# Performance work log

Measured on AMD Instinct MI355X. Metric: run time of the kernel, lower is better.

The kernel has to match this reference:

```python
import jax, jax.numpy as jnp
import numpy as np

B, H, W, C = 2, 128, 128, 256
D = 64          # attention_dim
NH = 1          # num_heads
P = 18          # num_random_points
N = H * W
EPS = 1e-5


def _layernorm(x, gamma, beta):
    mu = jnp.mean(x, axis=-1, keepdims=True)
    var = jnp.var(x, axis=-1, keepdims=True)
    return (x - mu) * jax.lax.rsqrt(var + EPS) * gamma + beta


def setup_inputs() -> dict:
    key = jax.random.key(0)
    ks = jax.random.split(key, 12)
    s = 0.02
    inp = {
        "X": jax.random.normal(ks[0], (B, H, W, C), dtype=jnp.float32),
        "selected_indices": jax.random.randint(ks[1], (B, N, P), 0, N),
        "topk": 1,
        "pos_enc": jax.random.normal(ks[2], (1, H, W, C), dtype=jnp.float32),
        "Wq": jax.random.normal(ks[3], (C, NH * D), dtype=jnp.float32) * s,
        "bq": jnp.zeros((NH * D,), dtype=jnp.float32),
        "Wk": jax.random.normal(ks[4], (C, NH * D), dtype=jnp.float32) * s,
        "bk": jnp.zeros((NH * D,), dtype=jnp.float32),
        "Wv": jax.random.normal(ks[5], (C, NH * D), dtype=jnp.float32) * s,
        "bv": jnp.zeros((NH * D,), dtype=jnp.float32),
        "Wo": jax.random.normal(ks[6], (NH * D, C), dtype=jnp.float32) * s,
        "bo": jnp.zeros((C,), dtype=jnp.float32),
        "W1": jax.random.normal(ks[7], (C, 4 * C), dtype=jnp.float32) * s,
        "b1": jnp.zeros((4 * C,), dtype=jnp.float32),
        "W2": jax.random.normal(ks[8], (4 * C, C), dtype=jnp.float32) * s,
        "b2": jnp.zeros((C,), dtype=jnp.float32),
        "g1": jnp.ones((C,), dtype=jnp.float32),
        "be1": jnp.zeros((C,), dtype=jnp.float32),
        "g2": jnp.ones((C,), dtype=jnp.float32),
        "be2": jnp.zeros((C,), dtype=jnp.float32),
    }
    return inp


def reference(X, selected_indices, topk, pos_enc, Wq, bq, Wk, bk, Wv, bv,
              Wo, bo, W1, b1, W2, b2, g1, be1, g2, be2):
    # forward_wotopk path (topk == 1)
    Xp = X + pos_enc                                  # [B,H,W,C]
    Q = (Xp @ Wq + bq).reshape(B, N, NH, D)
    K = (Xp @ Wk + bk).reshape(B, N, NH, D)
    V = (Xp @ Wv + bv).reshape(B, N, NH, D)

    # gather 18 random K/V rows per query pixel: [B,N,P,NH,D]
    gather = jax.vmap(lambda kv, idx: kv[idx])        # per-batch fancy index
    Ksel = gather(K, selected_indices)
    Vsel = gather(V, selected_indices)

    scores = jnp.einsum('bihd,bijhd->bijh', Q, Ksel) / jnp.sqrt(
        jnp.asarray(D, dtype=jnp.float32))
    attn = jax.nn.softmax(scores, axis=2)             # softmax over the P points
    ctx = jnp.einsum('bijh,bijhd->bihd', attn, Vsel).reshape(B, N, NH * D)

    out = (ctx @ Wo + bo).reshape(B, H, W, C)
    Xn = _layernorm(Xp + out, g1, be1)
    ffn = jax.nn.relu(Xn @ W1 + b1) @ W2 + b2
    out2 = _layernorm(Xn + ffn, g2, be2)
    return out2, attn
```

## Files before the change

### kernel.cpp

```cpp
#include <hip/hip_runtime.h>
#include <hip/hip_bf16.h>

#define CC 256
#define DD 64
#define PP 18
#define ROWS 32768
#define EPSF 1e-5f

typedef __attribute__((ext_vector_type(8))) short bf16x8;
typedef __attribute__((ext_vector_type(4))) short s16x4;
typedef __attribute__((ext_vector_type(4))) float f32x4;

__global__ __launch_bounds__(256) void k_prep(
    const float* __restrict__ Wq, const float* __restrict__ Wk,
    const float* __restrict__ Wv, const float* __restrict__ Wo,
    const float* __restrict__ W1, const float* __restrict__ W2,
    __hip_bfloat16* __restrict__ WqP, __hip_bfloat16* __restrict__ WkP,
    __hip_bfloat16* __restrict__ WvP, __hip_bfloat16* __restrict__ WoP,
    __hip_bfloat16* __restrict__ W1T, __hip_bfloat16* __restrict__ W2T) {
    __shared__ float tile[32][33];
    const int b = blockIdx.x, t = threadIdx.x;
    if (b < 256) {
        int i = b * 256 + t;
        const float* src; __hip_bfloat16* dst; int K, N, j;
        if (i < 16384)      { src = Wq; dst = WqP; K = 256; N = 64;  j = i; }
        else if (i < 32768) { src = Wk; dst = WkP; K = 256; N = 64;  j = i - 16384; }
        else if (i < 49152) { src = Wv; dst = WvP; K = 256; N = 64;  j = i - 32768; }
        else                { src = Wo; dst = WoP; K = 64;  N = 256; j = i - 49152; }
        int e = j & 7, l = (j >> 3) & 63, rest = j >> 9;
        int KS = K >> 5;
        int ks = rest % KS, nt = rest / KS;
        int row = ks * 32 + (l >> 4) * 8 + e;
        int col = nt * 16 + (l & 15);
        dst[j] = __float2bfloat16(src[(long)row * N + col]);
        return;
    }
    const float* src; __hip_bfloat16* dst; int Nsrc, r0, c0, mode;
    if (b < 512) {
        int bb = b - 256;
        r0 = (bb >> 5) * 32; c0 = (bb & 31) * 32;
        src = W1; dst = W1T; Nsrc = 1024; mode = 0;
    } else {
        int bb = b - 512;
        r0 = (bb >> 3) * 32; c0 = (bb & 7) * 32;
        src = W2; dst = W2T; Nsrc = 256; mode = 1;
    }
#pragma unroll
    for (int i = 0; i < 4; ++i) {
        int idx = t + i * 256;
        int r = idx >> 5, c = idx & 31;
        tile[r][c] = src[(long)(r0 + r) * Nsrc + c0 + c];
    }
    __syncthreads();
#pragma unroll
    for (int i = 0; i < 4; ++i) {
        int idx = t + i * 256;
        int c2 = idx >> 5, r2 = idx & 31;
        long doff = (mode == 0) ? ((long)(c0 + c2) * 256 + r0 + r2)
                                : ((long)(c0 + c2) * 1024 + r0 + r2);
        dst[doff] = __float2bfloat16(tile[r2][c2]);
    }
}

__global__ __launch_bounds__(256) void k_qkv(
    const float4* __restrict__ X4, const float4* __restrict__ pe4,
    const __hip_bfloat16* __restrict__ WqP, const __hip_bfloat16* __restrict__ WkP,
    const __hip_bfloat16* __restrict__ WvP,
    const float* __restrict__ bq, const float* __restrict__ bk,
    const float* __restrict__ bv,
    __hip_bfloat16* __restrict__ Xpb,
    __hip_bfloat16* __restrict__ Qb, __hip_bfloat16* __restrict__ Kb,
    __hip_bfloat16* __restrict__ Vb) {
    __shared__ short Xs[32 * 256];
    const int t = threadIdx.x, w = t >> 6, l = t & 63;
    const int l15 = l & 15, lh = l >> 4;
    const int row0 = blockIdx.x * 32;

    for (int j = t; j < 2048; j += 256) {
        int r = j >> 6, c4 = j & 63;
        long g = row0 + r;
        float4 a = X4[(g << 6) + c4];
        float4 p = pe4[(long)((g & 16383) << 6) + c4];
        union { s16x4 v; __hip_bfloat16 h[4]; } u;
        u.h[0] = __float2bfloat16(a.x + p.x);
        u.h[1] = __float2bfloat16(a.y + p.y);
        u.h[2] = __float2bfloat16(a.z + p.z);
        u.h[3] = __float2bfloat16(a.w + p.w);
        int db = (r << 9) + (c4 << 3);
        db ^= (r & 7) << 4;
        *(s16x4*)((char*)Xs + db) = u.v;
        *(s16x4*)((char*)Xpb + (g << 9) + (c4 << 3)) = u.v;
    }
    __syncthreads();

    bf16x8 af[2][8];
#pragma unroll
    for (int ri = 0; ri < 2; ++ri)
#pragma unroll
        for (int ks = 0; ks < 8; ++ks) {
            int r = ri * 16 + l15;
            int db = (r << 9) + ks * 64 + lh * 16;
            db ^= (r & 7) << 4;
            af[ri][ks] = *(const bf16x8*)((const char*)Xs + db);
        }

    f32x4 acc[3][2];
#pragma unroll
    for (int j = 0; j < 3; ++j)
#pragma unroll
        for (int ri = 0; ri < 2; ++ri) acc[j][ri] = (f32x4)(0.f);

#pragma unroll
    for (int ks = 0; ks < 8; ++ks)
#pragma unroll
        for (int j = 0; j < 3; ++j) {
            int nt = w * 3 + j;
            const __hip_bfloat16* WP = (nt < 4) ? WqP : ((nt < 8) ? WkP : WvP);
            int ntl = nt & 3;
            bf16x8 b = *(const bf16x8*)(WP + (long)(((ntl * 8 + ks) << 6) + l) * 8);
#pragma unroll
            for (int ri = 0; ri < 2; ++ri)
                acc[j][ri] = __builtin_amdgcn_mfma_f32_16x16x32_bf16(
                    af[ri][ks], b, acc[j][ri], 0, 0, 0);
        }

#pragma unroll
    for (int j = 0; j < 3; ++j) {
        int nt = w * 3 + j;
        __hip_bfloat16* OP = (nt < 4) ? Qb : ((nt < 8) ? Kb : Vb);
        const float* BP = (nt < 4) ? bq : ((nt < 8) ? bk : bv);
        int col = (nt & 3) * 16 + l15;
        float bias = BP[col];
#pragma unroll
        for (int ri = 0; ri < 2; ++ri)
#pragma unroll
            for (int rg = 0; rg < 4; ++rg) {
                long row = row0 + ri * 16 + lh * 4 + rg;
                OP[row * DD + col] = __float2bfloat16(acc[j][ri][rg] + bias);
            }
    }
}

__global__ __launch_bounds__(256) void k_attn(const __hip_bfloat16* __restrict__ Q,
                                              const __hip_bfloat16* __restrict__ K,
                                              const __hip_bfloat16* __restrict__ V,
                                              const int* __restrict__ sel,
                                              __hip_bfloat16* __restrict__ ctx,
                                              float* __restrict__ attn_out) {
    const int wave  = threadIdx.x >> 6;
    const int lane  = threadIdx.x & 63;
    const int token = blockIdx.x * 4 + wave;
    const int b     = token >> 14;
    const int g = lane >> 3, s = lane & 7;

    const int* selp = sel + (long)token * PP;
    int sel_l = (lane < PP) ? selp[lane] : 0;

    float qf[8];
    {
        uint4 qv = *(const uint4*)(Q + (long)token * DD + s * 8);
        qf[0] = __uint_as_float(qv.x << 16);
        qf[1] = __uint_as_float(qv.x & 0xffff0000u);
        qf[2] = __uint_as_float(qv.y << 16);
        qf[3] = __uint_as_float(qv.y & 0xffff0000u);
        qf[4] = __uint_as_float(qv.z << 16);
        qf[5] = __uint_as_float(qv.z & 0xffff0000u);
        qf[6] = __uint_as_float(qv.w << 16);
        qf[7] = __uint_as_float(qv.w & 0xffff0000u);
    }

    const __hip_bfloat16* Kbase = K + (((long)b << 14) * DD);
    float sc[3];
    int idxs[3];
#pragma unroll
    for (int i = 0; i < 3; ++i) {
        int r = i * 8 + g;
        idxs[i] = __shfl(sel_l, r);
        uint4 kv = *(const uint4*)(Kbase + (long)idxs[i] * DD + s * 8);
        float part;
        part = qf[0] * __uint_as_float(kv.x << 16);
        part = fmaf(qf[1], __uint_as_float(kv.x & 0xffff0000u), part);
        part = fmaf(qf[2], __uint_as_float(kv.y << 16), part);
        part = fmaf(qf[3], __uint_as_float(kv.y & 0xffff0000u), part);
        part = fmaf(qf[4], __uint_as_float(kv.z << 16), part);
        part = fmaf(qf[5], __uint_as_float(kv.z & 0xffff0000u), part);
        part = fmaf(qf[6], __uint_as_float(kv.w << 16), part);
        part = fmaf(qf[7], __uint_as_float(kv.w & 0xffff0000u), part);
        part += __shfl_xor(part, 1);
        part += __shfl_xor(part, 2);
        part += __shfl_xor(part, 4);
        sc[i] = (r < PP) ? part * 0.125f : -1e30f;
    }

    float m = fmaxf(fmaxf(sc[0], sc[1]), sc[2]);
    m = fmaxf(m, __shfl_xor(m, 8));
    m = fmaxf(m, __shfl_xor(m, 16));
    m = fmaxf(m, __shfl_xor(m, 32));
    const float L2E = 1.4426950408889634f;
    float e0 = exp2f((sc[0] - m) * L2E);
    float e1 = exp2f((sc[1] - m) * L2E);
    float e2 = exp2f((sc[2] - m) * L2E);
    float dsum = e0 + e1 + e2;
    dsum += __shfl_xor(dsum, 8);
    dsum += __shfl_xor(dsum, 16);
    dsum += __shfl_xor(dsum, 32);
    float inv = 1.f / dsum;

    {
        int srcl = (lane & 7) << 3;
        float b0 = __shfl(e0, srcl);
        float b1 = __shfl(e1, srcl);
        float b2 = __shfl(e2, srcl);
        if (lane < PP) {
            float ev = (lane < 8) ? b0 : ((lane < 16) ? b1 : b2);
            attn_out[(long)token * PP + lane] = ev * inv;
        }
    }

    const __hip_bfloat16* Vbase = V + (((long)b << 14) * DD);
    float ca[8];
#pragma unroll
    for (int j = 0; j < 8; ++j) ca[j] = 0.f;
    float ev3[3] = {e0, e1, e2};
#pragma unroll
    for (int i = 0; i < 3; ++i) {
        uint4 vv = *(const uint4*)(Vbase + (long)idxs[i] * DD + s * 8);
        float e = ev3[i];
        ca[0] = fmaf(e, __uint_as_float(vv.x << 16), ca[0]);
        ca[1] = fmaf(e, __uint_as_float(vv.x & 0xffff0000u), ca[1]);
        ca[2] = fmaf(e, __uint_as_float(vv.y << 16), ca[2]);
        ca[3] = fmaf(e, __uint_as_float(vv.y & 0xffff0000u), ca[3]);
        ca[4] = fmaf(e, __uint_as_float(vv.z << 16), ca[4]);
        ca[5] = fmaf(e, __uint_as_float(vv.z & 0xffff0000u), ca[5]);
        ca[6] = fmaf(e, __uint_as_float(vv.w << 16), ca[6]);
        ca[7] = fmaf(e, __uint_as_float(vv.w & 0xffff0000u), ca[7]);
    }
#pragma unroll
    for (int o = 8; o <= 32; o <<= 1)
#pragma unroll
        for (int j = 0; j < 8; ++j) ca[j] += __shfl_xor(ca[j], o);
    if (g == 0) {
        union { bf16x8 v; __hip_bfloat16 h[8]; } u;
#pragma unroll
        for (int j = 0; j < 8; ++j) u.h[j] = __float2bfloat16(ca[j] * inv);
        *(bf16x8*)(ctx + (long)token * DD + s * 8) = u.v;
    }
}

__global__ __launch_bounds__(256) void k_projln(
    const __hip_bfloat16* __restrict__ ctx, const __hip_bfloat16* __restrict__ WoP,
    const float* __restrict__ bo, const float* __restrict__ g1,
    const float* __restrict__ be1,
    const __hip_bfloat16* __restrict__ Xpb, __hip_bfloat16* __restrict__ Xnb) {
    __shared__ short Cs[32 * 64];
    __shared__ float red[2][32][2];
    __shared__ float mrs[32][2];
    const int t = threadIdx.x, w = t >> 6, l = t & 63;
    const int l15 = l & 15, lh = l >> 4;
    const int row0 = blockIdx.x * 32;

    {
        int r = t >> 3, ch = t & 7;
        int db = (r << 7) + (ch << 4);
        db ^= (r & 7) << 4;
        *(bf16x8*)((char*)Cs + db) = *(const bf16x8*)(ctx + (long)(row0 + r) * DD + ch * 8);
    }
    __syncthreads();

    const int ri = w & 1, nh = w >> 1;

    bf16x8 af[2];
#pragma unroll
    for (int ks = 0; ks < 2; ++ks) {
        int r = ri * 16 + l15;
        int db = (r << 7) + ks * 64 + lh * 16;
        db ^= (r & 7) << 4;
        af[ks] = *(const bf16x8*)((const char*)Cs + db);
    }

    f32x4 acc[8];
#pragma unroll
    for (int j = 0; j < 8; ++j) acc[j] = (f32x4)(0.f);

#pragma unroll
    for (int ks = 0; ks < 2; ++ks)
#pragma unroll
        for (int j = 0; j < 8; ++j) {
            int nt = nh * 8 + j;
            bf16x8 b = *(const bf16x8*)(WoP + (long)(((nt * 2 + ks) << 6) + l) * 8);
            acc[j] = __builtin_amdgcn_mfma_f32_16x16x32_bf16(af[ks], b, acc[j], 0, 0, 0);
        }

    float bov[8], g1v[8], be1v[8];
#pragma unroll
    for (int j = 0; j < 8; ++j) {
        int col = (nh * 8 + j) * 16 + l15;
        bov[j] = bo[col]; g1v[j] = g1[col]; be1v[j] = be1[col];
    }

    float xv[4][8];
#pragma unroll
    for (int rg = 0; rg < 4; ++rg) {
        long grow = row0 + ri * 16 + lh * 4 + rg;
        float s = 0.f, q = 0.f;
#pragma unroll
        for (int j = 0; j < 8; ++j) {
            float v = acc[j][rg] + bov[j] +
                      __bfloat162float(Xpb[grow * CC + (nh * 8 + j) * 16 + l15]);
            xv[rg][j] = v; s += v; q += v * v;
        }
#pragma unroll
        for (int o = 8; o > 0; o >>= 1) { s += __shfl_xor(s, o); q += __shfl_xor(q, o); }
        if (l15 == 0) {
            int rl = ri * 16 + lh * 4 + rg;
            red[nh][rl][0] = s; red[nh][rl][1] = q;
        }
    }
    __syncthreads();
    if (t < 32) {
        float S = red[0][t][0] + red[1][t][0];
        float Q = red[0][t][1] + red[1][t][1];
        float mu = S * (1.f / CC);
        float var = Q * (1.f / CC) - mu * mu;
        mrs[t][0] = mu; mrs[t][1] = rsqrtf(var + EPSF);
    }
    __syncthreads();
#pragma unroll
    for (int rg = 0; rg < 4; ++rg) {
        int rl = ri * 16 + lh * 4 + rg;
        long grow = row0 + rl;
        float mu = mrs[rl][0], rs = mrs[rl][1];
#pragma unroll
        for (int j = 0; j < 8; ++j)
            Xnb[grow * CC + (nh * 8 + j) * 16 + l15] =
                __float2bfloat16((xv[rg][j] - mu) * rs * g1v[j] + be1v[j]);
    }
}

template<int KD, int NDIM, int GRL2, int CTL2>
__global__ __launch_bounds__(256) void k_gemm(
    const __hip_bfloat16* __restrict__ A,
    const __hip_bfloat16* __restrict__ BT,
    const float* __restrict__ bias,
    __hip_bfloat16* __restrict__ Cout) {
    __shared__ short As[4096];
    __shared__ short Bs[4096];

    const int t = threadIdx.x, w = t >> 6, l = t & 63;
    const int l15 = l & 15, lh = l >> 4;
    const int bid = blockIdx.x;
    const int wi = bid & ((1 << (GRL2 + CTL2)) - 1);
    const int rt = ((bid >> (GRL2 + CTL2)) << GRL2) | (wi & ((1 << GRL2) - 1));
    const int ct = wi >> GRL2;
    const int row0 = rt * 128, n0 = ct * 128;
    const int wr = w & 1, wc = w >> 1;

    const int ar = t >> 2;
    const int ak = (t & 3) << 3;
    const int dbase = (ar * 64 + ((t & 3) << 4)) ^ ((ar & 7) << 4);
    const __hip_bfloat16* Ap = A + (long)(row0 + ar) * KD + ak;
    const __hip_bfloat16* Bp = BT + (long)(n0 + ar) * KD + ak;

    bf16x8 ra0 = *(const bf16x8*)(Ap);
    bf16x8 ra1 = *(const bf16x8*)(Ap + (long)64 * KD);
    bf16x8 rb0 = *(const bf16x8*)(Bp);
    bf16x8 rb1 = *(const bf16x8*)(Bp + (long)64 * KD);

    int offA[4], offB[4];
#pragma unroll
    for (int f = 0; f < 4; ++f) {
        int rowA = wr * 64 + f * 16 + l15;
        offA[f] = (rowA * 64 + lh * 16) ^ ((rowA & 7) << 4);
        int rowB = wc * 64 + f * 16 + l15;
        offB[f] = (rowB * 64 + lh * 16) ^ ((rowB & 7) << 4);
    }

    f32x4 acc[4][4];
#pragma unroll
    for (int i = 0; i < 4; ++i)
#pragma unroll
        for (int j = 0; j < 4; ++j) acc[i][j] = (f32x4)(0.f);

    constexpr int KS = KD / 32;
#pragma unroll 1
    for (int ks = 0; ks < KS; ++ks) {
        __syncthreads();
        *(bf16x8*)((char*)As + dbase)        = ra0;
        *(bf16x8*)((char*)As + 4096 + dbase) = ra1;
        *(bf16x8*)((char*)Bs + dbase)        = rb0;
        *(bf16x8*)((char*)Bs + 4096 + dbase) = rb1;
        if (ks + 1 < KS) {
            const __hip_bfloat16* Ap2 = Ap + (ks + 1) * 32;
            const __hip_bfloat16* Bp2 = Bp + (ks + 1) * 32;
            ra0 = *(const bf16x8*)(Ap2);
            ra1 = *(const bf16x8*)(Ap2 + (long)64 * KD);
            rb0 = *(const bf16x8*)(Bp2);
            rb1 = *(const bf16x8*)(Bp2 + (long)64 * KD);
        }
        __syncthreads();
        bf16x8 af[4], bfr[4];
#pragma unroll
        for (int f = 0; f < 4; ++f)
            af[f] = *(const bf16x8*)((const char*)As + offA[f]);
#pragma unroll
        for (int f = 0; f < 4; ++f)
            bfr[f] = *(const bf16x8*)((const char*)Bs + offB[f]);
#pragma unroll
        for (int fr = 0; fr < 4; ++fr)
#pragma unroll
            for (int fc = 0; fc < 4; ++fc)
                acc[fr][fc] = __builtin_amdgcn_mfma_f32_16x16x32_bf16(
                    af[fr], bfr[fc], acc[fr][fc], 0, 0, 0);
    }

#pragma unroll
    for (int fc = 0; fc < 4; ++fc) {
        int col = n0 + wc * 64 + fc * 16 + l15;
        float bv = bias[col];
#pragma unroll
        for (int fr = 0; fr < 4; ++fr)
#pragma unroll
            for (int rg = 0; rg < 4; ++rg) {
                int row = wr * 64 + fr * 16 + lh * 4 + rg;
                long gi = (long)(row0 + row) * NDIM + col;
                Cout[gi] = __float2bfloat16(fmaxf(acc[fr][fc][rg] + bv, 0.f));
            }
    }
}

__global__ __launch_bounds__(512) void k_gemm2ln(
    const __hip_bfloat16* __restrict__ A,
    const __hip_bfloat16* __restrict__ BT,
    const float* __restrict__ b2,
    const __hip_bfloat16* __restrict__ Res,
    const float* __restrict__ g2, const float* __restrict__ be2,
    float* __restrict__ out) {
    __shared__ short As[4096];
    __shared__ short Bs[8192];
    __shared__ float red[4][128][2];
    __shared__ float mrs[128][2];

    const int t = threadIdx.x, w = t >> 6, l = t & 63;
    const int l15 = l & 15, lh = l >> 4;
    const int wr = w >> 2, wc = w & 3;
    const int row0 = blockIdx.x * 128;

    const int ar = t >> 2;
    const int ak = (t & 3) << 3;
    const int dbA  = (ar * 64 + ((t & 3) << 4)) ^ ((ar & 7) << 4);
    const int br1  = ar + 128;
    const int dbB0 = dbA;
    const int dbB1 = (br1 * 64 + ((t & 3) << 4)) ^ ((br1 & 7) << 4);
    const __hip_bfloat16* Ap  = A  + (long)(row0 + ar) * 1024 + ak;
    const __hip_bfloat16* Bp0 = BT + (long)ar  * 1024 + ak;
    const __hip_bfloat16* Bp1 = BT + (long)br1 * 1024 + ak;

    bf16x8 ra  = *(const bf16x8*)(Ap);
    bf16x8 rb0 = *(const bf16x8*)(Bp0);
    bf16x8 rb1 = *(const bf16x8*)(Bp1);

    int offA[4], offB[4];
#pragma unroll
    for (int f = 0; f < 4; ++f) {
        int rowA = wr * 64 + f * 16 + l15;
        offA[f] = (rowA * 64 + lh * 16) ^ ((rowA & 7) << 4);
        int rowB = wc * 64 + f * 16 + l15;
        offB[f] = (rowB * 64 + lh * 16) ^ ((rowB & 7) << 4);
    }

    f32x4 acc[4][4];
#pragma unroll
    for (int i = 0; i < 4; ++i)
#pragma unroll
        for (int j = 0; j < 4; ++j) acc[i][j] = (f32x4)(0.f);

#pragma unroll 1
    for (int ks = 0; ks < 32; ++ks) {
        __syncthreads();
        *(bf16x8*)((char*)As + dbA)  = ra;
        *(bf16x8*)((char*)Bs + dbB0) = rb0;
        *(bf16x8*)((char*)Bs + dbB1) = rb1;
        if (ks + 1 < 32) {
            ra  = *(const bf16x8*)(Ap  + (ks + 1) * 32);
            rb0 = *(const bf16x8*)(Bp0 + (ks + 1) * 32);
            rb1 = *(const bf16x8*)(Bp1 + (ks + 1) * 32);
        }
        __syncthreads();
        bf16x8 af[4], bfr[4];
#pragma unroll
        for (int f = 0; f < 4; ++f)
            af[f] = *(const bf16x8*)((const char*)As + offA[f]);
#pragma unroll
        for (int f = 0; f < 4; ++f)
            bfr[f] = *(const bf16x8*)((const char*)Bs + offB[f]);
#pragma unroll
        for (int fr = 0; fr < 4; ++fr)
#pragma unroll
            for (int fc = 0; fc < 4; ++fc)
                acc[fr][fc] = __builtin_amdgcn_mfma_f32_16x16x32_bf16(
                    af[fr], bfr[fc], acc[fr][fc], 0, 0, 0);
    }

    float b2v[4], g2v[4], be2v[4];
#pragma unroll
    for (int fc = 0; fc < 4; ++fc) {
        int col = wc * 64 + fc * 16 + l15;
        b2v[fc] = b2[col]; g2v[fc] = g2[col]; be2v[fc] = be2[col];
    }
#pragma unroll
    for (int fr = 0; fr < 4; ++fr)
#pragma unroll
        for (int rg = 0; rg < 4; ++rg) {
            int row = wr * 64 + fr * 16 + lh * 4 + rg;
            float s = 0.f, q = 0.f;
#pragma unroll
            for (int fc = 0; fc < 4; ++fc) {
                long gi = (long)(row0 + row) * CC + wc * 64 + fc * 16 + l15;
                float v = acc[fr][fc][rg] + b2v[fc] + __bfloat162float(Res[gi]);
                acc[fr][fc][rg] = v;
                s += v; q += v * v;
            }
#pragma unroll
            for (int o = 8; o > 0; o >>= 1) {
                s += __shfl_xor(s, o); q += __shfl_xor(q, o);
            }
            if (l15 == 0) { red[wc][row][0] = s; red[wc][row][1] = q; }
        }
    __syncthreads();
    if (t < 128) {
        float S = 0.f, Q = 0.f;
#pragma unroll
        for (int ww = 0; ww < 4; ++ww) { S += red[ww][t][0]; Q += red[ww][t][1]; }
        float mu = S * (1.f / CC);
        float var = Q * (1.f / CC) - mu * mu;
        mrs[t][0] = mu; mrs[t][1] = rsqrtf(var + EPSF);
    }
    __syncthreads();
#pragma unroll
    for (int fr = 0; fr < 4; ++fr)
#pragma unroll
        for (int rg = 0; rg < 4; ++rg) {
            int row = wr * 64 + fr * 16 + lh * 4 + rg;
            float mu = mrs[row][0], rs = mrs[row][1];
#pragma unroll
            for (int fc = 0; fc < 4; ++fc) {
                long gi = (long)(row0 + row) * CC + wc * 64 + fc * 16 + l15;
                out[gi] = (acc[fr][fc][rg] - mu) * rs * g2v[fc] + be2v[fc];
            }
        }
}

extern "C" void kernel_launch(void* const* d_in, const int* in_sizes, int n_in,
                              void* d_out, int out_size, void* d_ws, size_t ws_size,
                              hipStream_t stream) {
    const float* X   = (const float*)d_in[0];
    const int*   sel = (const int*)d_in[1];
    const float* pe  = (const float*)d_in[3];
    const float* Wq  = (const float*)d_in[4];
    const float* bq  = (const float*)d_in[5];
    const float* Wk  = (const float*)d_in[6];
    const float* bk  = (const float*)d_in[7];
    const float* Wv  = (const float*)d_in[8];
    const float* bv  = (const float*)d_in[9];
    const float* Wo  = (const float*)d_in[10];
    const float* bo  = (const float*)d_in[11];
    const float* W1  = (const float*)d_in[12];
    const float* b1  = (const float*)d_in[13];
    const float* W2  = (const float*)d_in[14];
    const float* b2  = (const float*)d_in[15];
    const float* g1  = (const float*)d_in[16];
    const float* be1 = (const float*)d_in[17];
    const float* g2  = (const float*)d_in[18];
    const float* be2 = (const float*)d_in[19];

    float* out = (float*)d_out;
    char*  ws  = (char*)d_ws;

    __hip_bfloat16* Xpb = (__hip_bfloat16*)(ws);
    __hip_bfloat16* Qb  = (__hip_bfloat16*)(ws + (16 << 20));
    __hip_bfloat16* Kb  = (__hip_bfloat16*)(ws + (20 << 20));
    __hip_bfloat16* Vb  = (__hip_bfloat16*)(ws + (24 << 20));
    __hip_bfloat16* ctxb= (__hip_bfloat16*)(ws + (28 << 20));
    __hip_bfloat16* H   = (__hip_bfloat16*)(ws + (16 << 20));
    __hip_bfloat16* WqP = (__hip_bfloat16*)(ws + (96 << 20));
    __hip_bfloat16* WkP = WqP + 16384;
    __hip_bfloat16* WvP = WkP + 16384;
    __hip_bfloat16* WoP = WvP + 16384;
    __hip_bfloat16* W1T = WoP + 16384;
    __hip_bfloat16* W2T = W1T + 262144;
    float* attn_out = out + (long)ROWS * CC;

    k_prep<<<768, 256, 0, stream>>>(Wq, Wk, Wv, Wo, W1, W2,
                                    WqP, WkP, WvP, WoP, W1T, W2T);

    k_qkv<<<ROWS / 32, 256, 0, stream>>>((const float4*)X, (const float4*)pe,
                                         WqP, WkP, WvP, bq, bk, bv,
                                         Xpb, Qb, Kb, Vb);

    k_attn<<<ROWS / 4, 256, 0, stream>>>(Qb, Kb, Vb, sel, ctxb, attn_out);

    k_projln<<<ROWS / 32, 256, 0, stream>>>(ctxb, WoP, bo, g1, be1, Xpb, Xpb);

    k_gemm<256, 1024, 3, 3><<<2048, 256, 0, stream>>>(Xpb, W1T, b1, H);
    k_gemm2ln<<<256, 512, 0, stream>>>(H, W2T, b2, Xpb, g2, be2, out);
}
```

Measured before the change: 120.1 us.

## Fuse FFN up and down GEMMs into one kernel with hidden tile in LDS

Replaces the separate W1 GEMM (writing a bf16 hidden buffer to global memory) and the W2+LayerNorm GEMM with a single kernel. Each 64-row block computes its full 1024-wide hidden activation into 128KB of shared memory, then runs the down projection and LayerNorm from there. Weights are now prepacked into MFMA fragment order so they load straight from global memory without LDS staging. This removes the global round trip of the hidden tensor and one launch. In exchange it uses a large LDS footprint that allows only one block per CU and rereads all weights for every row block.

Measured after the change: 113.8 us. 1.05x faster.

```diff
diff --git a/kernel.cpp b/kernel.cpp
--- a/kernel.cpp
+++ b/kernel.cpp
@@ -17,49 +17,26 @@
     const float* __restrict__ W1, const float* __restrict__ W2,
     __hip_bfloat16* __restrict__ WqP, __hip_bfloat16* __restrict__ WkP,
     __hip_bfloat16* __restrict__ WvP, __hip_bfloat16* __restrict__ WoP,
-    __hip_bfloat16* __restrict__ W1T, __hip_bfloat16* __restrict__ W2T) {
-    __shared__ float tile[32][33];
+    __hip_bfloat16* __restrict__ W1P, __hip_bfloat16* __restrict__ W2P) {
     const int b = blockIdx.x, t = threadIdx.x;
+    const float* src; __hip_bfloat16* dst; int K, N, j;
     if (b < 256) {
         int i = b * 256 + t;
-        const float* src; __hip_bfloat16* dst; int K, N, j;
         if (i < 16384)      { src = Wq; dst = WqP; K = 256; N = 64;  j = i; }
         else if (i < 32768) { src = Wk; dst = WkP; K = 256; N = 64;  j = i - 16384; }
         else if (i < 49152) { src = Wv; dst = WvP; K = 256; N = 64;  j = i - 32768; }
         else                { src = Wo; dst = WoP; K = 64;  N = 256; j = i - 49152; }
-        int e = j & 7, l = (j >> 3) & 63, rest = j >> 9;
-        int KS = K >> 5;
-        int ks = rest % KS, nt = rest / KS;
-        int row = ks * 32 + (l >> 4) * 8 + e;
-        int col = nt * 16 + (l & 15);
-        dst[j] = __float2bfloat16(src[(long)row * N + col]);
-        return;
-    }
-    const float* src; __hip_bfloat16* dst; int Nsrc, r0, c0, mode;
-    if (b < 512) {
-        int bb = b - 256;
-        r0 = (bb >> 5) * 32; c0 = (bb & 31) * 32;
-        src = W1; dst = W1T; Nsrc = 1024; mode = 0;
+    } else if (b < 1280) {
+        src = W1; dst = W1P; K = 256;  N = 1024; j = (b - 256) * 256 + t;
     } else {
-        int bb = b - 512;
-        r0 = (bb >> 3) * 32; c0 = (bb & 7) * 32;
-        src = W2; dst = W2T; Nsrc = 256; mode = 1;
-    }
-#pragma unroll
-    for (int i = 0; i < 4; ++i) {
-        int idx = t + i * 256;
-        int r = idx >> 5, c = idx & 31;
-        tile[r][c] = src[(long)(r0 + r) * Nsrc + c0 + c];
-    }
-    __syncthreads();
-#pragma unroll
-    for (int i = 0; i < 4; ++i) {
-        int idx = t + i * 256;
-        int c2 = idx >> 5, r2 = idx & 31;
-        long doff = (mode == 0) ? ((long)(c0 + c2) * 256 + r0 + r2)
-                                : ((long)(c0 + c2) * 1024 + r0 + r2);
-        dst[doff] = __float2bfloat16(tile[r2][c2]);
-    }
+        src = W2; dst = W2P; K = 1024; N = 256;  j = (b - 1280) * 256 + t;
+    }
+    int e = j & 7, l = (j >> 3) & 63, rest = j >> 9;
+    int KS = K >> 5;
+    int ks = rest % KS, nt = rest / KS;
+    int row = ks * 32 + (l >> 4) * 8 + e;
+    int col = nt * 16 + (l & 15);
+    dst[j] = __float2bfloat16(src[(long)row * N + col]);
 }
 
 __global__ __launch_bounds__(256) void k_qkv(
@@ -337,215 +314,155 @@
     }
 }
 
-template<int KD, int NDIM, int GRL2, int CTL2>
-__global__ __launch_bounds__(256) void k_gemm(
-    const __hip_bfloat16* __restrict__ A,
-    const __hip_bfloat16* __restrict__ BT,
-    const float* __restrict__ bias,
-    __hip_bfloat16* __restrict__ Cout) {
-    __shared__ short As[4096];
-    __shared__ short Bs[4096];
+__global__ __launch_bounds__(512) void k_ffn(
+    const __hip_bfloat16* __restrict__ Xn,
+    const __hip_bfloat16* __restrict__ W1P,
+    const float* __restrict__ b1,
+    const __hip_bfloat16* __restrict__ W2P,
+    const float* __restrict__ b2,
+    const float* __restrict__ g2, const float* __restrict__ be2,
+    float* __restrict__ out) {
+    __shared__ short Hs[64 * 1024];
+    __shared__ float red[8][64][2];
+    __shared__ float mrs[64][2];
 
     const int t = threadIdx.x, w = t >> 6, l = t & 63;
     const int l15 = l & 15, lh = l >> 4;
-    const int bid = blockIdx.x;
-    const int wi = bid & ((1 << (GRL2 + CTL2)) - 1);
-    const int rt = ((bid >> (GRL2 + CTL2)) << GRL2) | (wi & ((1 << GRL2) - 1));
-    const int ct = wi >> GRL2;
-    const int row0 = rt * 128, n0 = ct * 128;
-    const int wr = w & 1, wc = w >> 1;
-
-    const int ar = t >> 2;
-    const int ak = (t & 3) << 3;
-    const int dbase = (ar * 64 + ((t & 3) << 4)) ^ ((ar & 7) << 4);
-    const __hip_bfloat16* Ap = A + (long)(row0 + ar) * KD + ak;
-    const __hip_bfloat16* Bp = BT + (long)(n0 + ar) * KD + ak;
-
-    bf16x8 ra0 = *(const bf16x8*)(Ap);
-    bf16x8 ra1 = *(const bf16x8*)(Ap + (long)64 * KD);
-    bf16x8 rb0 = *(const bf16x8*)(Bp);
-    bf16x8 rb1 = *(const bf16x8*)(Bp + (long)64 * KD);
-
-    int offA[4], offB[4];
+    const int row0 = blockIdx.x * 64;
+
+    {
+        f32x4 hacc[8][4];
+#pragma unroll
+        for (int a = 0; a < 8; ++a)
+#pragma unroll
+            for (int f = 0; f < 4; ++f) hacc[a][f] = (f32x4)(0.f);
+
+        const __hip_bfloat16* xb = Xn + (long)(row0 + l15) * CC + lh * 8;
+
+#pragma unroll
+        for (int ks = 0; ks < 8; ++ks) {
+            bf16x8 afr[8];
+#pragma unroll
+            for (int a = 0; a < 8; ++a)
+                afr[a] = *(const bf16x8*)(
+                    W1P + (long)((((w * 8 + a) * 8 + ks) << 6) + l) * 8);
+            bf16x8 xfr[4];
+#pragma unroll
+            for (int f = 0; f < 4; ++f)
+                xfr[f] = *(const bf16x8*)(xb + f * 16 * CC + ks * 32);
+#pragma unroll
+            for (int a = 0; a < 8; ++a)
+#pragma unroll
+                for (int f = 0; f < 4; ++f)
+                    hacc[a][f] = __builtin_amdgcn_mfma_f32_16x16x32_bf16(
+                        afr[a], xfr[f], hacc[a][f], 0, 0, 0);
+        }
+
+#pragma unroll
+        for (int a = 0; a < 8; ++a) {
+            int hid4 = w * 128 + a * 16 + lh * 4;
+            float4 b1q = *(const float4*)(b1 + hid4);
+#pragma unroll
+            for (int f = 0; f < 4; ++f) {
+                int xrow = f * 16 + l15;
+                union { s16x4 v; __hip_bfloat16 h[4]; } u;
+                u.h[0] = __float2bfloat16(fmaxf(hacc[a][f][0] + b1q.x, 0.f));
+                u.h[1] = __float2bfloat16(fmaxf(hacc[a][f][1] + b1q.y, 0.f));
+                u.h[2] = __float2bfloat16(fmaxf(hacc[a][f][2] + b1q.z, 0.f));
+                u.h[3] = __float2bfloat16(fmaxf(hacc[a][f][3] + b1q.w, 0.f));
+                int db = (xrow << 11) + ((hid4 * 2) ^ ((xrow & 7) << 4));
+                *(s16x4*)((char*)Hs + db) = u.v;
+            }
+        }
+    }
+    __syncthreads();
+
+    f32x4 acc[4][2];
+#pragma unroll
+    for (int f = 0; f < 4; ++f)
+#pragma unroll
+        for (int j = 0; j < 2; ++j) acc[f][j] = (f32x4)(0.f);
+
+    int offH[4][2];
 #pragma unroll
     for (int f = 0; f < 4; ++f) {
-        int rowA = wr * 64 + f * 16 + l15;
-        offA[f] = (rowA * 64 + lh * 16) ^ ((rowA & 7) << 4);
-        int rowB = wc * 64 + f * 16 + l15;
-        offB[f] = (rowB * 64 + lh * 16) ^ ((rowB & 7) << 4);
-    }
-
-    f32x4 acc[4][4];
-#pragma unroll
-    for (int i = 0; i < 4; ++i)
-#pragma unroll
-        for (int j = 0; j < 4; ++j) acc[i][j] = (f32x4)(0.f);
-
-    constexpr int KS = KD / 32;
-#pragma unroll 1
-    for (int ks = 0; ks < KS; ++ks) {
-        __syncthreads();
-        *(bf16x8*)((char*)As + dbase)        = ra0;
-        *(bf16x8*)((char*)As + 4096 + dbase) = ra1;
-        *(bf16x8*)((char*)Bs + dbase)        = rb0;
-        *(bf16x8*)((char*)Bs + 4096 + dbase) = rb1;
-        if (ks + 1 < KS) {
-            const __hip_bfloat16* Ap2 = Ap + (ks + 1) * 32;
-            const __hip_bfloat16* Bp2 = Bp + (ks + 1) * 32;
-            ra0 = *(const bf16x8*)(Ap2);
-            ra1 = *(const bf16x8*)(Ap2 + (long)64 * KD);
-            rb0 = *(const bf16x8*)(Bp2);
-            rb1 = *(const bf16x8*)(Bp2 + (long)64 * KD);
-        }
-        __syncthreads();
-        bf16x8 af[4], bfr[4];
+        int rowA = f * 16 + l15;
+        int sw = (rowA & 7) << 4;
+#pragma unroll
+        for (int kk = 0; kk < 2; ++kk)
+            offH[f][kk] = (rowA << 11) + (((kk * 64 + lh * 16)) ^ sw);
+    }
+
+#pragma unroll 2
+    for (int ks = 0; ks < 16; ++ks) {
+        bf16x8 bfr[2][2];
+#pragma unroll
+        for (int j = 0; j < 2; ++j)
+#pragma unroll
+            for (int kk = 0; kk < 2; ++kk)
+                bfr[j][kk] = *(const bf16x8*)(
+                    W2P + (long)((((w * 2 + j) * 32 + ks * 2 + kk) << 6) + l) * 8);
+        bf16x8 afr[4][2];
 #pragma unroll
         for (int f = 0; f < 4; ++f)
-            af[f] = *(const bf16x8*)((const char*)As + offA[f]);
-#pragma unroll
-        for (int f = 0; f < 4; ++f)
-            bfr[f] = *(const bf16x8*)((const char*)Bs + offB[f]);
-#pragma unroll
-        for (int fr = 0; fr < 4; ++fr)
-#pragma unroll
-            for (int fc = 0; fc < 4; ++fc)
-                acc[fr][fc] = __builtin_amdgcn_mfma_f32_16x16x32_bf16(
-                    af[fr], bfr[fc], acc[fr][fc], 0, 0, 0);
-    }
-
-#pragma unroll
-    for (int fc = 0; fc < 4; ++fc) {
-        int col = n0 + wc * 64 + fc * 16 + l15;
-        float bv = bias[col];
-#pragma unroll
-        for (int fr = 0; fr < 4; ++fr)
-#pragma unroll
-            for (int rg = 0; rg < 4; ++rg) {
-                int row = wr * 64 + fr * 16 + lh * 4 + rg;
-                long gi = (long)(row0 + row) * NDIM + col;
-                Cout[gi] = __float2bfloat16(fmaxf(acc[fr][fc][rg] + bv, 0.f));
-            }
-    }
-}
-
-__global__ __launch_bounds__(512) void k_gemm2ln(
-    const __hip_bfloat16* __restrict__ A,
-    const __hip_bfloat16* __restrict__ BT,
-    const float* __restrict__ b2,
-    const __hip_bfloat16* __restrict__ Res,
-    const float* __restrict__ g2, const float* __restrict__ be2,
-    float* __restrict__ out) {
-    __shared__ short As[4096];
-    __shared__ short Bs[8192];
-    __shared__ float red[4][128][2];
-    __shared__ float mrs[128][2];
-
-    const int t = threadIdx.x, w = t >> 6, l = t & 63;
-    const int l15 = l & 15, lh = l >> 4;
-    const int wr = w >> 2, wc = w & 3;
-    const int row0 = blockIdx.x * 128;
-
-    const int ar = t >> 2;
-    const int ak = (t & 3) << 3;
-    const int dbA  = (ar * 64 + ((t & 3) << 4)) ^ ((ar & 7) << 4);
-    const int br1  = ar + 128;
-    const int dbB0 = dbA;
-    const int dbB1 = (br1 * 64 + ((t & 3) << 4)) ^ ((br1 & 7) << 4);
-    const __hip_bfloat16* Ap  = A  + (long)(row0 + ar) * 1024 + ak;
-    const __hip_bfloat16* Bp0 = BT + (long)ar  * 1024 + ak;
-    const __hip_bfloat16* Bp1 = BT + (long)br1 * 1024 + ak;
-
-    bf16x8 ra  = *(const bf16x8*)(Ap);
-    bf16x8 rb0 = *(const bf16x8*)(Bp0);
-    bf16x8 rb1 = *(const bf16x8*)(Bp1);
-
-    int offA[4], offB[4];
-#pragma unroll
-    for (int f = 0; f < 4; ++f) {
-        int rowA = wr * 64 + f * 16 + l15;
-        offA[f] = (rowA * 64 + lh * 16) ^ ((rowA & 7) << 4);
-        int rowB = wc * 64 + f * 16 + l15;
-        offB[f] = (rowB * 64 + lh * 16) ^ ((rowB & 7) << 4);
-    }
-
-    f32x4 acc[4][4];
-#pragma unroll
-    for (int i = 0; i < 4; ++i)
-#pragma unroll
-        for (int j = 0; j < 4; ++j) acc[i][j] = (f32x4)(0.f);
-
-#pragma unroll 1
-    for (int ks = 0; ks < 32; ++ks) {
-        __syncthreads();
-        *(bf16x8*)((char*)As + dbA)  = ra;
-        *(bf16x8*)((char*)Bs + dbB0) = rb0;
-        *(bf16x8*)((char*)Bs + dbB1) = rb1;
-        if (ks + 1 < 32) {
-            ra  = *(const bf16x8*)(Ap  + (ks + 1) * 32);
-            rb0 = *(const bf16x8*)(Bp0 + (ks + 1) * 32);
-            rb1 = *(const bf16x8*)(Bp1 + (ks + 1) * 32);
-        }
-        __syncthreads();
-        bf16x8 af[4], bfr[4];
-#pragma unroll
-        for (int f = 0; f < 4; ++f)
-            af[f] = *(const bf16x8*)((const char*)As + offA[f]);
-#pragma unroll
-        for (int f = 0; f < 4; ++f)
-            bfr[f] = *(const bf16x8*)((const char*)Bs + offB[f]);
-#pragma unroll
-        for (int fr = 0; fr < 4; ++fr)
-#pragma unroll
-            for (int fc = 0; fc < 4; ++fc)
-                acc[fr][fc] = __builtin_amdgcn_mfma_f32_16x16x32_bf16(
-                    af[fr], bfr[fc], acc[fr][fc], 0, 0, 0);
-    }
-
-    float b2v[4], g2v[4], be2v[4];
-#pragma unroll
-    for (int fc = 0; fc < 4; ++fc) {
-        int col = wc * 64 + fc * 16 + l15;
-        b2v[fc] = b2[col]; g2v[fc] = g2[col]; be2v[fc] = be2[col];
-    }
-#pragma unroll
-    for (int fr = 0; fr < 4; ++fr)
+#pragma unroll
+            for (int kk = 0; kk < 2; ++kk)
+                afr[f][kk] = *(const bf16x8*)((const char*)Hs + offH[f][kk] + ks * 128);
+#pragma unroll
+        for (int kk = 0; kk < 2; ++kk)
+#pragma unroll
+            for (int f = 0; f < 4; ++f)
+#pragma unroll
+                for (int j = 0; j < 2; ++j)
+                    acc[f][j] = __builtin_amdgcn_mfma_f32_16x16x32_bf16(
+                        afr[f][kk], bfr[j][kk], acc[f][j], 0, 0, 0);
+    }
+
+    float b2v[2], g2v[2], be2v[2];
+#pragma unroll
+    for (int j = 0; j < 2; ++j) {
+        int col = w * 32 + j * 16 + l15;
+        b2v[j] = b2[col]; g2v[j] = g2[col]; be2v[j] = be2[col];
+    }
+#pragma unroll
+    for (int f = 0; f < 4; ++f)
 #pragma unroll
         for (int rg = 0; rg < 4; ++rg) {
-            int row = wr * 64 + fr * 16 + lh * 4 + rg;
+            int row = f * 16 + lh * 4 + rg;
             float s = 0.f, q = 0.f;
 #pragma unroll
-            for (int fc = 0; fc < 4; ++fc) {
-                long gi = (long)(row0 + row) * CC + wc * 64 + fc * 16 + l15;
-                float v = acc[fr][fc][rg] + b2v[fc] + __bfloat162float(Res[gi]);
-                acc[fr][fc][rg] = v;
+            for (int j = 0; j < 2; ++j) {
+                long gi = (long)(row0 + row) * CC + w * 32 + j * 16 + l15;
+                float v = acc[f][j][rg] + b2v[j] + __bfloat162float(Xn[gi]);
+                acc[f][j][rg] = v;
                 s += v; q += v * v;
             }
 #pragma unroll
             for (int o = 8; o > 0; o >>= 1) {
                 s += __shfl_xor(s, o); q += __shfl_xor(q, o);
             }
-            if (l15 == 0) { red[wc][row][0] = s; red[wc][row][1] = q; }
-        }
-    __syncthreads();
-    if (t < 128) {
+            if (l15 == 0) { red[w][row][0] = s; red[w][row][1] = q; }
+        }
+    __syncthreads();
+    if (t < 64) {
         float S = 0.f, Q = 0.f;
 #pragma unroll
-        for (int ww = 0; ww < 4; ++ww) { S += red[ww][t][0]; Q += red[ww][t][1]; }
+        for (int ww = 0; ww < 8; ++ww) { S += red[ww][t][0]; Q += red[ww][t][1]; }
         float mu = S * (1.f / CC);
         float var = Q * (1.f / CC) - mu * mu;
         mrs[t][0] = mu; mrs[t][1] = rsqrtf(var + EPSF);
     }
     __syncthreads();
 #pragma unroll
-    for (int fr = 0; fr < 4; ++fr)
+    for (int f = 0; f < 4; ++f)
 #pragma unroll
         for (int rg = 0; rg < 4; ++rg) {
-            int row = wr * 64 + fr * 16 + lh * 4 + rg;
+            int row = f * 16 + lh * 4 + rg;
             float mu = mrs[row][0], rs = mrs[row][1];
 #pragma unroll
-            for (int fc = 0; fc < 4; ++fc) {
-                long gi = (long)(row0 + row) * CC + wc * 64 + fc * 16 + l15;
-                out[gi] = (acc[fr][fc][rg] - mu) * rs * g2v[fc] + be2v[fc];
+            for (int j = 0; j < 2; ++j) {
+                long gi = (long)(row0 + row) * CC + w * 32 + j * 16 + l15;
+                out[gi] = (acc[f][j][rg] - mu) * rs * g2v[j] + be2v[j];
             }
         }
 }
@@ -581,17 +498,16 @@
     __hip_bfloat16* Kb  = (__hip_bfloat16*)(ws + (20 << 20));
     __hip_bfloat16* Vb  = (__hip_bfloat16*)(ws + (24 << 20));
     __hip_bfloat16* ctxb= (__hip_bfloat16*)(ws + (28 << 20));
-    __hip_bfloat16* H   = (__hip_bfloat16*)(ws + (16 << 20));
     __hip_bfloat16* WqP = (__hip_bfloat16*)(ws + (96 << 20));
     __hip_bfloat16* WkP = WqP + 16384;
     __hip_bfloat16* WvP = WkP + 16384;
     __hip_bfloat16* WoP = WvP + 16384;
-    __hip_bfloat16* W1T = WoP + 16384;
-    __hip_bfloat16* W2T = W1T + 262144;
+    __hip_bfloat16* W1P = WoP + 16384;
+    __hip_bfloat16* W2P = W1P + 262144;
     float* attn_out = out + (long)ROWS * CC;
 
-    k_prep<<<768, 256, 0, stream>>>(Wq, Wk, Wv, Wo, W1, W2,
-                                    WqP, WkP, WvP, WoP, W1T, W2T);
+    k_prep<<<2304, 256, 0, stream>>>(Wq, Wk, Wv, Wo, W1, W2,
+                                     WqP, WkP, WvP, WoP, W1P, W2P);
 
     k_qkv<<<ROWS / 32, 256, 0, stream>>>((const float4*)X, (const float4*)pe,
                                          WqP, WkP, WvP, bq, bk, bv,
@@ -601,6 +517,5 @@
 
     k_projln<<<ROWS / 32, 256, 0, stream>>>(ctxb, WoP, bo, g1, be1, Xpb, Xpb);
 
-    k_gemm<256, 1024, 3, 3><<<2048, 256, 0, stream>>>(Xpb, W1T, b1, H);
-    k_gemm2ln<<<256, 512, 0, stream>>>(H, W2T, b2, Xpb, g2, be2, out);
+    k_ffn<<<ROWS / 64, 512, 0, stream>>>(Xpb, W1P, b1, W2P, b2, g2, be2, out);
 }
```
